# Optimization experiments

Measured on AMD Instinct MI355X. Metric: run time of the kernel, lower is better.

Reference implementation:

```python
import jax, jax.numpy as jnp
import numpy as np

N_HEAD = 8
ALPHA = 5.0
EPS = 1e-12  # matches F.normalize default


def setup_inputs() -> dict:
    key = jax.random.key(0)
    kq, kk, kv = jax.random.split(key, 3)
    B, D, T = 4, 1024, 2048
    q = jax.random.normal(kq, (B, D, T), dtype=jnp.float32)
    k = jax.random.normal(kk, (B, D, T), dtype=jnp.float32)
    v = jax.random.normal(kv, (B, D, T), dtype=jnp.float32)
    return {"q": q, "k": k, "v": v}


def _l2norm(x, axis):
    n = jnp.sqrt(jnp.sum(x * x, axis=axis, keepdims=True))
    return x / jnp.maximum(n, EPS)


def reference(q, k, v):
    B, D, Tq = q.shape
    Tk = k.shape[-1]
    Dv = v.shape[-2]
    h = N_HEAD
    d = D // h
    dv = Dv // h
    qh = q.reshape(B, h, d, Tq)
    kh = k.reshape(B, h, d, Tk)
    vh = v.reshape(B, h, dv, Tk)
    # cosine-normalize over per-head channel dim (axis -2)
    qn = _l2norm(qh, axis=-2)
    kn = _l2norm(kh, axis=-2)
    qk = ALPHA * jnp.einsum('bhdq,bhdk->bhqk', qn, kn)
    sm = jax.nn.softmax(qk, axis=-1)
    # (sm.unsqueeze(-3) * v.unsqueeze(-2)).sum(-1)  ==  einsum over k
    out = jnp.einsum('bhqk,bhdk->bhdq', sm, vh)
    return out.reshape(B, Dv, Tq)
```

## Files before the change

kernel.cpp:

```cpp
#include <hip/hip_runtime.h>


#define T_SEQ 2048
#define DH 128
#define BH 32

typedef float f32x4 __attribute__((ext_vector_type(4)));
typedef __bf16 bf16x8 __attribute__((ext_vector_type(8)));
typedef __bf16 bf16x4 __attribute__((ext_vector_type(4)));

__device__ __forceinline__ void async_copy16(const void* g, void* l) {
  __builtin_amdgcn_global_load_lds(
      (const __attribute__((address_space(1))) void*)g,
      (__attribute__((address_space(3))) void*)l, 16, 0, 0);
}

__global__ __launch_bounds__(256) void prepass_kernel(
    const float* __restrict__ ksrc, const float* __restrict__ vsrc,
    __bf16* __restrict__ kn, __bf16* __restrict__ vb) {
  __shared__ float tile[64 * 133];
  __shared__ float part[4][64];
  __shared__ float inv_t[64];
  const int tid = threadIdx.x;

  if (blockIdx.x >= 1024) {
    int i = (blockIdx.x - 1024) * 256 + tid;
    f32x4 a = *(const f32x4*)(vsrc + (size_t)i * 8);
    f32x4 b = *(const f32x4*)(vsrc + (size_t)i * 8 + 4);
    bf16x8 ob;
    ob[0] = (__bf16)a[0]; ob[1] = (__bf16)a[1]; ob[2] = (__bf16)a[2]; ob[3] = (__bf16)a[3];
    ob[4] = (__bf16)b[0]; ob[5] = (__bf16)b[1]; ob[6] = (__bf16)b[2]; ob[7] = (__bf16)b[3];
    *(bf16x8*)(vb + (size_t)i * 8) = ob;
    return;
  }

  const int bh = blockIdx.x >> 5;
  const int t0 = (blockIdx.x & 31) * 64;
#pragma unroll
  for (int it = 0; it < 8; ++it) {
    int c = it * 256 + tid;
    int ch = c >> 4;
    int t4 = (c & 15) * 4;
    f32x4 v = *(const f32x4*)(ksrc + (size_t)(bh * DH + ch) * T_SEQ + t0 + t4);
#pragma unroll
    for (int i = 0; i < 4; ++i) tile[(t4 + i) * 133 + ch] = v[i];
  }
  __syncthreads();
  const int t = tid & 63;
  const int seg = tid >> 6;
  float ss = 0.f;
#pragma unroll
  for (int i = 0; i < 8; ++i) {
    f32x4 x = *(const f32x4*)(tile + t * 133 + seg * 32 + i * 4);
    ss += x[0]*x[0] + x[1]*x[1] + x[2]*x[2] + x[3]*x[3];
  }
  part[seg][t] = ss;
  __syncthreads();
  if (tid < 64) {
    float n = sqrtf(part[0][tid] + part[1][tid] + part[2][tid] + part[3][tid]);
    inv_t[tid] = 1.f / fmaxf(n, 1e-12f);
  }
  __syncthreads();
  const int t_o = tid >> 2;
  const int c0 = (tid & 3) * 32;
  const float inv = inv_t[t_o];
  __bf16* drow = kn + (size_t)(bh * T_SEQ + t0 + t_o) * DH + c0;
#pragma unroll
  for (int cc = 0; cc < 4; ++cc) {
    f32x4 a = *(const f32x4*)(tile + t_o * 133 + c0 + cc * 8);
    f32x4 b = *(const f32x4*)(tile + t_o * 133 + c0 + cc * 8 + 4);
    bf16x8 ob;
    ob[0] = (__bf16)(a[0]*inv); ob[1] = (__bf16)(a[1]*inv);
    ob[2] = (__bf16)(a[2]*inv); ob[3] = (__bf16)(a[3]*inv);
    ob[4] = (__bf16)(b[0]*inv); ob[5] = (__bf16)(b[1]*inv);
    ob[6] = (__bf16)(b[2]*inv); ob[7] = (__bf16)(b[3]*inv);
    *(bf16x8*)(drow + cc * 8) = ob;
  }
}

__device__ __forceinline__ void stage_tiles(
    const __bf16* kbase, const __bf16* vbase, __bf16* lk, __bf16* lv,
    int koff, int w, int qi, int g) {
#pragma unroll
  for (int i = 0; i < 4; ++i) {
    const int f = w * 4 + i;
    const int mt = f >> 2, s = f & 3;
    async_copy16(kbase + (size_t)(koff + mt * 16 + qi) * DH + s * 32 + g * 8,
                 lk + f * 512);
  }
#pragma unroll
  for (int i = 0; i < 4; ++i) {
    const int f = w * 4 + i;
    const int mt = f >> 1, st = f & 1;
    async_copy16(vbase + (size_t)(mt * 16 + qi) * T_SEQ + koff + st * 32 + g * 8,
                 lv + f * 512);
  }
}

__global__ __launch_bounds__(256, 2) void attn_kernel(
    const float* __restrict__ q, const __bf16* __restrict__ kn,
    const __bf16* __restrict__ vb, float* __restrict__ out) {
  __shared__ __align__(16) __bf16 lds_k[2][16 * 512];
  __shared__ __align__(16) __bf16 lds_v[2][16 * 512];
  __shared__ __align__(16) __bf16 p_buf[8 * 1024];

  const int bh = blockIdx.x >> 4;
  const int q0 = (blockIdx.x & 15) * 128;
  const int tid = threadIdx.x;
  const int w = tid >> 6, lane = tid & 63;
  const int qi = lane & 15, g = lane >> 4;

  const __bf16* kbase = kn + (size_t)bh * (T_SEQ * DH);
  const __bf16* vbase = vb + (size_t)bh * (DH * T_SEQ);
  const float* qsrc = q + (size_t)bh * (DH * T_SEQ);

  stage_tiles(kbase, vbase, lds_k[0], lds_v[0], 0, w, qi, g);

  bf16x8 qf[2][4];
#pragma unroll
  for (int nt = 0; nt < 2; ++nt) {
    const int t = q0 + w * 32 + nt * 16 + qi;
    float xv[32];
    float ss = 0.f;
#pragma unroll
    for (int s = 0; s < 4; ++s)
#pragma unroll
      for (int j = 0; j < 8; ++j) {
        float x = qsrc[(size_t)(s * 32 + g * 8 + j) * T_SEQ + t];
        xv[s * 8 + j] = x;
        ss += x * x;
      }
    ss += __shfl_xor(ss, 16, 64);
    ss += __shfl_xor(ss, 32, 64);
    const float inv = 5.0f / fmaxf(sqrtf(ss), 1e-12f);
#pragma unroll
    for (int s = 0; s < 4; ++s) {
      bf16x8 f;
#pragma unroll
      for (int j = 0; j < 8; ++j) f[j] = (__bf16)(xv[s * 8 + j] * inv);
      qf[nt][s] = f;
    }
  }

  f32x4 o_acc[2][8];
#pragma unroll
  for (int nt = 0; nt < 2; ++nt)
#pragma unroll
    for (int i = 0; i < 8; ++i) o_acc[nt][i] = (f32x4)(0.f);
  float lsum[2] = {0.f, 0.f};

  const int swz = (qi & 7) << 3;
  __bf16* pw0 = p_buf + (w * 2 + 0) * 1024 + qi * 64;
  __bf16* pw1 = p_buf + (w * 2 + 1) * 1024 + qi * 64;

  for (int it = 0; it < 32; ++it) {
    __syncthreads();
    const int cur = it & 1;
    if (it + 1 < 32)
      stage_tiles(kbase, vbase, lds_k[cur ^ 1], lds_v[cur ^ 1],
                  (it + 1) * 64, w, qi, g);

    const __bf16* lk = lds_k[cur];
    f32x4 sacc[2][4];
#pragma unroll
    for (int nt = 0; nt < 2; ++nt)
#pragma unroll
      for (int mt = 0; mt < 4; ++mt) sacc[nt][mt] = (f32x4)(0.f);
#pragma unroll
    for (int s = 0; s < 4; ++s)
#pragma unroll
      for (int mt = 0; mt < 4; ++mt) {
        bf16x8 a = *(const bf16x8*)(lk + ((mt * 4 + s) * 64 + lane) * 8);
        sacc[0][mt] = __builtin_amdgcn_mfma_f32_16x16x32_bf16(a, qf[0][s], sacc[0][mt], 0, 0, 0);
        sacc[1][mt] = __builtin_amdgcn_mfma_f32_16x16x32_bf16(a, qf[1][s], sacc[1][mt], 0, 0, 0);
      }

#pragma unroll
    for (int nt = 0; nt < 2; ++nt) {
      __bf16* pw = nt ? pw1 : pw0;
      float rs = 0.f;
#pragma unroll
      for (int mt = 0; mt < 4; ++mt) {
        bf16x4 pb;
#pragma unroll
        for (int r = 0; r < 4; ++r) {
          float e = __expf(sacc[nt][mt][r]);
          rs += e;
          pb[r] = (__bf16)e;
        }
        *(bf16x4*)(pw + ((mt * 16 + g * 4) ^ swz)) = pb;
      }
      lsum[nt] += rs;
    }

    const __bf16* lv = lds_v[cur];
#pragma unroll
    for (int st = 0; st < 2; ++st) {
      bf16x8 pf0 = *(const bf16x8*)(pw0 + ((st * 32 + g * 8) ^ swz));
      bf16x8 pf1 = *(const bf16x8*)(pw1 + ((st * 32 + g * 8) ^ swz));
#pragma unroll
      for (int mt = 0; mt < 8; ++mt) {
        bf16x8 a = *(const bf16x8*)(lv + ((mt * 2 + st) * 64 + lane) * 8);
        o_acc[0][mt] = __builtin_amdgcn_mfma_f32_16x16x32_bf16(a, pf0, o_acc[0][mt], 0, 0, 0);
        o_acc[1][mt] = __builtin_amdgcn_mfma_f32_16x16x32_bf16(a, pf1, o_acc[1][mt], 0, 0, 0);
      }
    }
  }

#pragma unroll
  for (int nt = 0; nt < 2; ++nt) {
    float l = lsum[nt];
    l += __shfl_xor(l, 16, 64);
    l += __shfl_xor(l, 32, 64);
    const float rinv = 1.f / l;
    const int tq = q0 + w * 32 + nt * 16 + qi;
#pragma unroll
    for (int mt = 0; mt < 8; ++mt)
#pragma unroll
      for (int r = 0; r < 4; ++r)
        out[(size_t)(bh * DH + mt * 16 + g * 4 + r) * T_SEQ + tq] =
            o_acc[nt][mt][r] * rinv;
  }
}

extern "C" void kernel_launch(void* const* d_in, const int* in_sizes, int n_in,
                              void* d_out, int out_size, void* d_ws, size_t ws_size,
                              hipStream_t stream) {
  const float* q = (const float*)d_in[0];
  const float* k = (const float*)d_in[1];
  const float* v = (const float*)d_in[2];
  float* out = (float*)d_out;
  const size_t n = (size_t)BH * T_SEQ * DH;
  if (ws_size < 2 * n * sizeof(__bf16)) return;
  __bf16* kn = (__bf16*)d_ws;
  __bf16* vbf = kn + n;

  prepass_kernel<<<dim3(1024 + 4096), dim3(256), 0, stream>>>(k, v, kn, vbf);
  attn_kernel<<<dim3(512), dim3(256), 0, stream>>>(q, kn, vbf, out);
}
```

Before: 214.7 us.

## Fuse V bf16 conversion into attention kernel with register-staged prefetch

```diff
diff --git a/kernel.cpp b/kernel.cpp
--- a/kernel.cpp
+++ b/kernel.cpp
@@ -15,72 +15,51 @@
       (__attribute__((address_space(3))) void*)l, 16, 0, 0);
 }
 
-__global__ __launch_bounds__(256) void prepass_kernel(
-    const float* __restrict__ ksrc, const float* __restrict__ vsrc,
-    __bf16* __restrict__ kn, __bf16* __restrict__ vb) {
-  __shared__ float tile[64 * 133];
+__global__ __launch_bounds__(256) void prepass_k_kernel(
+    const float* __restrict__ ksrc, __bf16* __restrict__ kn) {
   __shared__ float part[4][64];
-  __shared__ float inv_t[64];
-  const int tid = threadIdx.x;
-
-  if (blockIdx.x >= 1024) {
-    int i = (blockIdx.x - 1024) * 256 + tid;
-    f32x4 a = *(const f32x4*)(vsrc + (size_t)i * 8);
-    f32x4 b = *(const f32x4*)(vsrc + (size_t)i * 8 + 4);
-    bf16x8 ob;
-    ob[0] = (__bf16)a[0]; ob[1] = (__bf16)a[1]; ob[2] = (__bf16)a[2]; ob[3] = (__bf16)a[3];
-    ob[4] = (__bf16)b[0]; ob[5] = (__bf16)b[1]; ob[6] = (__bf16)b[2]; ob[7] = (__bf16)b[3];
-    *(bf16x8*)(vb + (size_t)i * 8) = ob;
-    return;
-  }
-
+  __shared__ float inv_s[64];
+  __shared__ __bf16 tile[64 * 136];
   const int bh = blockIdx.x >> 5;
   const int t0 = (blockIdx.x & 31) * 64;
-#pragma unroll
-  for (int it = 0; it < 8; ++it) {
-    int c = it * 256 + tid;
-    int ch = c >> 4;
-    int t4 = (c & 15) * 4;
-    f32x4 v = *(const f32x4*)(ksrc + (size_t)(bh * DH + ch) * T_SEQ + t0 + t4);
-#pragma unroll
-    for (int i = 0; i < 4; ++i) tile[(t4 + i) * 133 + ch] = v[i];
-  }
-  __syncthreads();
+  const int tid = threadIdx.x;
+  const int seg = tid >> 6;
   const int t = tid & 63;
-  const int seg = tid >> 6;
+
+  const float* src = ksrc + (size_t)bh * DH * T_SEQ + t0 + t;
+  float x[32];
   float ss = 0.f;
 #pragma unroll
-  for (int i = 0; i < 8; ++i) {
-    f32x4 x = *(const f32x4*)(tile + t * 133 + seg * 32 + i * 4);
-    ss += x[0]*x[0] + x[1]*x[1] + x[2]*x[2] + x[3]*x[3];
+  for (int i = 0; i < 32; ++i) {
+    x[i] = src[(size_t)(seg * 32 + i) * T_SEQ];
+    ss += x[i] * x[i];
   }
   part[seg][t] = ss;
   __syncthreads();
   if (tid < 64) {
     float n = sqrtf(part[0][tid] + part[1][tid] + part[2][tid] + part[3][tid]);
-    inv_t[tid] = 1.f / fmaxf(n, 1e-12f);
+    inv_s[tid] = 1.f / fmaxf(n, 1e-12f);
   }
   __syncthreads();
-  const int t_o = tid >> 2;
+  const float inv = inv_s[t];
+#pragma unroll
+  for (int o = 0; o < 4; ++o) {
+    bf16x8 ob;
+#pragma unroll
+    for (int j = 0; j < 8; ++j) ob[j] = (__bf16)(x[o * 8 + j] * inv);
+    *(bf16x8*)(tile + t * 136 + seg * 32 + o * 8) = ob;
+  }
+  __syncthreads();
+  const int t2 = tid >> 2;
   const int c0 = (tid & 3) * 32;
-  const float inv = inv_t[t_o];
-  __bf16* drow = kn + (size_t)(bh * T_SEQ + t0 + t_o) * DH + c0;
-#pragma unroll
-  for (int cc = 0; cc < 4; ++cc) {
-    f32x4 a = *(const f32x4*)(tile + t_o * 133 + c0 + cc * 8);
-    f32x4 b = *(const f32x4*)(tile + t_o * 133 + c0 + cc * 8 + 4);
-    bf16x8 ob;
-    ob[0] = (__bf16)(a[0]*inv); ob[1] = (__bf16)(a[1]*inv);
-    ob[2] = (__bf16)(a[2]*inv); ob[3] = (__bf16)(a[3]*inv);
-    ob[4] = (__bf16)(b[0]*inv); ob[5] = (__bf16)(b[1]*inv);
-    ob[6] = (__bf16)(b[2]*inv); ob[7] = (__bf16)(b[3]*inv);
-    *(bf16x8*)(drow + cc * 8) = ob;
-  }
-}
-
-__device__ __forceinline__ void stage_tiles(
-    const __bf16* kbase, const __bf16* vbase, __bf16* lk, __bf16* lv,
-    int koff, int w, int qi, int g) {
+  __bf16* drow = kn + (size_t)(bh * T_SEQ + t0 + t2) * DH + c0;
+#pragma unroll
+  for (int cc = 0; cc < 4; ++cc)
+    *(bf16x8*)(drow + cc * 8) = *(const bf16x8*)(tile + t2 * 136 + c0 + cc * 8);
+}
+
+__device__ __forceinline__ void stage_k(
+    const __bf16* kbase, __bf16* lk, int koff, int w, int qi, int g) {
 #pragma unroll
   for (int i = 0; i < 4; ++i) {
     const int f = w * 4 + i;
@@ -88,18 +67,36 @@
     async_copy16(kbase + (size_t)(koff + mt * 16 + qi) * DH + s * 32 + g * 8,
                  lk + f * 512);
   }
-#pragma unroll
-  for (int i = 0; i < 4; ++i) {
-    const int f = w * 4 + i;
-    const int mt = f >> 1, st = f & 1;
-    async_copy16(vbase + (size_t)(mt * 16 + qi) * T_SEQ + koff + st * 32 + g * 8,
-                 lv + f * 512);
+}
+
+__device__ __forceinline__ void stage_v_loads(
+    const float* vsrc, int k0, int tid, f32x4* x) {
+#pragma unroll
+  for (int i = 0; i < 8; ++i) {
+    const int c = i * 256 + tid;
+    const int ch = c >> 4, t4 = (c & 15) * 4;
+    x[i] = *(const f32x4*)(vsrc + (size_t)ch * T_SEQ + k0 + t4);
+  }
+}
+
+__device__ __forceinline__ void stage_v_write(
+    __bf16* lv, int tid, const f32x4* x) {
+#pragma unroll
+  for (int i = 0; i < 8; ++i) {
+    const int c = i * 256 + tid;
+    const int ch = c >> 4, t4 = (c & 15) * 4;
+    const int f = ((ch >> 4) << 1) + (t4 >> 5);
+    const int idx = f * 512 + ((((t4 & 31) >> 3) * 16 + (ch & 15)) << 3) + (t4 & 7);
+    bf16x4 ob;
+    ob[0] = (__bf16)x[i][0]; ob[1] = (__bf16)x[i][1];
+    ob[2] = (__bf16)x[i][2]; ob[3] = (__bf16)x[i][3];
+    *(bf16x4*)(lv + idx) = ob;
   }
 }
 
 __global__ __launch_bounds__(256, 2) void attn_kernel(
     const float* __restrict__ q, const __bf16* __restrict__ kn,
-    const __bf16* __restrict__ vb, float* __restrict__ out) {
+    const float* __restrict__ v, float* __restrict__ out) {
   __shared__ __align__(16) __bf16 lds_k[2][16 * 512];
   __shared__ __align__(16) __bf16 lds_v[2][16 * 512];
   __shared__ __align__(16) __bf16 p_buf[8 * 1024];
@@ -111,10 +108,12 @@
   const int qi = lane & 15, g = lane >> 4;
 
   const __bf16* kbase = kn + (size_t)bh * (T_SEQ * DH);
-  const __bf16* vbase = vb + (size_t)bh * (DH * T_SEQ);
+  const float* vsrc = v + (size_t)bh * (DH * T_SEQ);
   const float* qsrc = q + (size_t)bh * (DH * T_SEQ);
 
-  stage_tiles(kbase, vbase, lds_k[0], lds_v[0], 0, w, qi, g);
+  f32x4 vx[8];
+  stage_k(kbase, lds_k[0], 0, w, qi, g);
+  stage_v_loads(vsrc, 0, tid, vx);
 
   bf16x8 qf[2][4];
 #pragma unroll
@@ -126,9 +125,9 @@
     for (int s = 0; s < 4; ++s)
 #pragma unroll
       for (int j = 0; j < 8; ++j) {
-        float x = qsrc[(size_t)(s * 32 + g * 8 + j) * T_SEQ + t];
-        xv[s * 8 + j] = x;
-        ss += x * x;
+        float xq = qsrc[(size_t)(s * 32 + g * 8 + j) * T_SEQ + t];
+        xv[s * 8 + j] = xq;
+        ss += xq * xq;
       }
     ss += __shfl_xor(ss, 16, 64);
     ss += __shfl_xor(ss, 32, 64);
@@ -141,6 +140,7 @@
       qf[nt][s] = f;
     }
   }
+  stage_v_write(lds_v[0], tid, vx);
 
   f32x4 o_acc[2][8];
 #pragma unroll
@@ -156,9 +156,11 @@
   for (int it = 0; it < 32; ++it) {
     __syncthreads();
     const int cur = it & 1;
-    if (it + 1 < 32)
-      stage_tiles(kbase, vbase, lds_k[cur ^ 1], lds_v[cur ^ 1],
-                  (it + 1) * 64, w, qi, g);
+    const bool pf = (it + 1 < 32);
+    if (pf) {
+      stage_k(kbase, lds_k[cur ^ 1], (it + 1) * 64, w, qi, g);
+      stage_v_loads(vsrc, (it + 1) * 64, tid, vx);
+    }
 
     const __bf16* lk = lds_k[cur];
     f32x4 sacc[2][4];
@@ -205,6 +207,8 @@
         o_acc[1][mt] = __builtin_amdgcn_mfma_f32_16x16x32_bf16(a, pf1, o_acc[1][mt], 0, 0, 0);
       }
     }
+
+    if (pf) stage_v_write(lds_v[cur ^ 1], tid, vx);
   }
 
 #pragma unroll
@@ -231,10 +235,9 @@
   const float* v = (const float*)d_in[2];
   float* out = (float*)d_out;
   const size_t n = (size_t)BH * T_SEQ * DH;
-  if (ws_size < 2 * n * sizeof(__bf16)) return;
+  if (ws_size < n * sizeof(__bf16)) return;
   __bf16* kn = (__bf16*)d_ws;
-  __bf16* vbf = kn + n;
-
-  prepass_kernel<<<dim3(1024 + 4096), dim3(256), 0, stream>>>(k, v, kn, vbf);
-  attn_kernel<<<dim3(512), dim3(256), 0, stream>>>(q, kn, vbf, out);
-}
+
+  prepass_k_kernel<<<dim3(1024), dim3(256), 0, stream>>>(k, kn);
+  attn_kernel<<<dim3(512), dim3(256), 0, stream>>>(q, kn, v, out);
+}
```

Result: slower. 226.8 us (+5.6%).

## Stream K prepass through registers with bf16 tile and remap attention blocks

Applied to the files above, without the earlier changes.

```diff
diff --git a/kernel.cpp b/kernel.cpp
--- a/kernel.cpp
+++ b/kernel.cpp
@@ -18,9 +18,9 @@
 __global__ __launch_bounds__(256) void prepass_kernel(
     const float* __restrict__ ksrc, const float* __restrict__ vsrc,
     __bf16* __restrict__ kn, __bf16* __restrict__ vb) {
-  __shared__ float tile[64 * 133];
   __shared__ float part[4][64];
-  __shared__ float inv_t[64];
+  __shared__ float inv_s[64];
+  __shared__ __bf16 tile[64 * 136];
   const int tid = threadIdx.x;
 
   if (blockIdx.x >= 1024) {
@@ -36,46 +36,39 @@
 
   const int bh = blockIdx.x >> 5;
   const int t0 = (blockIdx.x & 31) * 64;
-#pragma unroll
-  for (int it = 0; it < 8; ++it) {
-    int c = it * 256 + tid;
-    int ch = c >> 4;
-    int t4 = (c & 15) * 4;
-    f32x4 v = *(const f32x4*)(ksrc + (size_t)(bh * DH + ch) * T_SEQ + t0 + t4);
-#pragma unroll
-    for (int i = 0; i < 4; ++i) tile[(t4 + i) * 133 + ch] = v[i];
-  }
-  __syncthreads();
+  const int seg = tid >> 6;
   const int t = tid & 63;
-  const int seg = tid >> 6;
+
+  const float* src = ksrc + (size_t)bh * DH * T_SEQ + t0 + t;
+  float x[32];
   float ss = 0.f;
 #pragma unroll
-  for (int i = 0; i < 8; ++i) {
-    f32x4 x = *(const f32x4*)(tile + t * 133 + seg * 32 + i * 4);
-    ss += x[0]*x[0] + x[1]*x[1] + x[2]*x[2] + x[3]*x[3];
+  for (int i = 0; i < 32; ++i) {
+    x[i] = src[(size_t)(seg * 32 + i) * T_SEQ];
+    ss += x[i] * x[i];
   }
   part[seg][t] = ss;
   __syncthreads();
   if (tid < 64) {
     float n = sqrtf(part[0][tid] + part[1][tid] + part[2][tid] + part[3][tid]);
-    inv_t[tid] = 1.f / fmaxf(n, 1e-12f);
+    inv_s[tid] = 1.f / fmaxf(n, 1e-12f);
   }
   __syncthreads();
-  const int t_o = tid >> 2;
+  const float inv = inv_s[t];
+#pragma unroll
+  for (int o = 0; o < 4; ++o) {
+    bf16x8 ob;
+#pragma unroll
+    for (int j = 0; j < 8; ++j) ob[j] = (__bf16)(x[o * 8 + j] * inv);
+    *(bf16x8*)(tile + t * 136 + seg * 32 + o * 8) = ob;
+  }
+  __syncthreads();
+  const int t2 = tid >> 2;
   const int c0 = (tid & 3) * 32;
-  const float inv = inv_t[t_o];
-  __bf16* drow = kn + (size_t)(bh * T_SEQ + t0 + t_o) * DH + c0;
-#pragma unroll
-  for (int cc = 0; cc < 4; ++cc) {
-    f32x4 a = *(const f32x4*)(tile + t_o * 133 + c0 + cc * 8);
-    f32x4 b = *(const f32x4*)(tile + t_o * 133 + c0 + cc * 8 + 4);
-    bf16x8 ob;
-    ob[0] = (__bf16)(a[0]*inv); ob[1] = (__bf16)(a[1]*inv);
-    ob[2] = (__bf16)(a[2]*inv); ob[3] = (__bf16)(a[3]*inv);
-    ob[4] = (__bf16)(b[0]*inv); ob[5] = (__bf16)(b[1]*inv);
-    ob[6] = (__bf16)(b[2]*inv); ob[7] = (__bf16)(b[3]*inv);
-    *(bf16x8*)(drow + cc * 8) = ob;
-  }
+  __bf16* drow = kn + (size_t)(bh * T_SEQ + t0 + t2) * DH + c0;
+#pragma unroll
+  for (int cc = 0; cc < 4; ++cc)
+    *(bf16x8*)(drow + cc * 8) = *(const bf16x8*)(tile + t2 * 136 + c0 + cc * 8);
 }
 
 __device__ __forceinline__ void stage_tiles(
@@ -104,8 +97,8 @@
   __shared__ __align__(16) __bf16 lds_v[2][16 * 512];
   __shared__ __align__(16) __bf16 p_buf[8 * 1024];
 
-  const int bh = blockIdx.x >> 4;
-  const int q0 = (blockIdx.x & 15) * 128;
+  const int bh = (blockIdx.x & 7) + ((blockIdx.x >> 3) & 3) * 8;
+  const int q0 = (blockIdx.x >> 5) * 128;
   const int tid = threadIdx.x;
   const int w = tid >> 6, lane = tid & 63;
   const int qi = lane & 15, g = lane >> 4;
@@ -126,9 +119,9 @@
     for (int s = 0; s < 4; ++s)
 #pragma unroll
       for (int j = 0; j < 8; ++j) {
-        float x = qsrc[(size_t)(s * 32 + g * 8 + j) * T_SEQ + t];
-        xv[s * 8 + j] = x;
-        ss += x * x;
+        float xq = qsrc[(size_t)(s * 32 + g * 8 + j) * T_SEQ + t];
+        xv[s * 8 + j] = xq;
+        ss += xq * xq;
       }
     ss += __shfl_xor(ss, 16, 64);
     ss += __shfl_xor(ss, 32, 64);
```

After: 211.4 us. About the same (-1.5%).
